# Performance work log

Measured on AMD Instinct MI355X. Metric: run time of the kernel, lower is better.

The kernel has to match this reference:

```python
import jax, jax.numpy as jnp
import numpy as np

WIN = 25            # window size (win_h == win_w == 25)
DIM = 256           # channels
DIM_HEAD = 32
HEADS = DIM // DIM_HEAD   # 8
HIDDEN = int(DIM * 2.0)   # mlp_ratio = 2.0
EPS = 1e-5


def _rel_pos_indices(w=WIN):
    # replicates the buffer built in Attention.__init__
    pos = np.arange(w)
    gi, gj = np.meshgrid(pos, pos, indexing='ij')
    grid = np.stack([gi.ravel(), gj.ravel()], axis=-1)          # (w*w, 2)
    rel = grid[:, None, :] - grid[None, :, :] + (w - 1)          # (n, n, 2)
    return jnp.asarray(rel[..., 0] * (2 * w - 1) + rel[..., 1])  # (n, n) int


def setup_inputs() -> dict:
    key = jax.random.key(0)
    ks = jax.random.split(key, 8)
    s = 0.02
    d = DIM
    return {
        'x': jax.random.normal(ks[0], (2, d, 100, 100), jnp.float32),
        'w_qkv': jax.random.normal(ks[1], (3 * d, d), jnp.float32) * s,
        'w_out': jax.random.normal(ks[2], (d, d), jnp.float32) * s,
        'rel_bias_table': jax.random.normal(ks[3], ((2 * WIN - 1) ** 2, HEADS), jnp.float32) * s,
        'gamma2': jnp.ones((d,), jnp.float32),
        'beta2': jnp.zeros((d,), jnp.float32),
        'w1': jax.random.normal(ks[4], (HIDDEN, d), jnp.float32) * s,
        'b1': jnp.zeros((HIDDEN,), jnp.float32),
        'w2': jax.random.normal(ks[5], (d, HIDDEN), jnp.float32) * s,
        'b2': jnp.zeros((d,), jnp.float32),
    }


def _layernorm(x, g, b, eps=EPS):
    m = x.mean(-1, keepdims=True)
    v = ((x - m) ** 2).mean(-1, keepdims=True)
    return (x - m) / jnp.sqrt(v + eps) * g + b


def reference(x, w_qkv, w_out, rel_bias_table, gamma2, beta2, w1, b1, w2, b2):
    b, d, H, W = x.shape
    nh, nw = H // WIN, W // WIN
    h, dh = HEADS, DIM_HEAD
    scale = dh ** -0.5
    n = WIN * WIN

    # --- window partition: (b, d, H, W) -> (b*nh*nw, n, d) ---
    xw = x.reshape(b, d, nh, WIN, nw, WIN).transpose(0, 2, 4, 3, 5, 1)
    xw = xw.reshape(b * nh * nw, n, d)

    # --- windowed attention with relative-position bias (norm1 unused in source) ---
    qkv = xw @ w_qkv.T                         # (B, n, 3d)
    q, k, v = jnp.split(qkv, 3, axis=-1)
    split_heads = lambda t: t.reshape(t.shape[0], n, h, dh).transpose(0, 2, 1, 3)
    q = split_heads(q) * scale                 # (B, h, n, dh)
    k = split_heads(k)
    v = split_heads(v)

    sim = jnp.einsum('bhid,bhjd->bhij', q, k)  # (B, h, n, n)
    bias = rel_bias_table[_rel_pos_indices()]  # (n, n, h)
    sim = sim + bias.transpose(2, 0, 1)[None]
    attn = jax.nn.softmax(sim, axis=-1)
    out = jnp.einsum('bhij,bhjd->bhid', attn, v)            # (B, h, n, dh)
    out = out.transpose(0, 2, 1, 3).reshape(-1, n, d)        # head-major concat: (m d)
    out = out @ w_out.T                                      # (B, n, d)

    # --- un-partition: (b*nh*nw, n, d) -> (b, d, H, W) ---
    xa = out.reshape(b, nh, nw, WIN, WIN, d).transpose(0, 5, 1, 3, 2, 4)
    xa = xa.reshape(b, d, H, W)

    # --- norm2 + MLP + residual ---
    y = xa.transpose(0, 2, 3, 1).reshape(b, H * W, d)
    y = _layernorm(y, gamma2, beta2)
    y = jax.nn.gelu(y @ w1.T + b1, approximate=False) @ w2.T + b2
    y = y.reshape(b, H, W, d).transpose(0, 3, 1, 2)
    return x + y
```

## Files before the change

### kernel.cpp

```cpp
#include <hip/hip_runtime.h>


using f32x4 = __attribute__((ext_vector_type(4))) float;
using s16x8 = __attribute__((ext_vector_type(8))) short;

__device__ __forceinline__ ushort f2b(float f) {
  union { float f; unsigned u; } v; v.f = f;
  return (ushort)((v.u + 0x7FFFu + ((v.u >> 16) & 1u)) >> 16);
}
__device__ __forceinline__ ushort f2b_fast(float f) {
  union { float f; unsigned u; } v; v.f = f;
  return (ushort)((v.u + 0x8000u) >> 16);
}
__device__ __forceinline__ float b2f(ushort u) {
  union { unsigned u; float f; } v; v.u = ((unsigned)u) << 16; return v.f;
}
__device__ __forceinline__ float lo2f(unsigned w) {
  union { unsigned u; float f; } v; v.u = w << 16; return v.f;
}
__device__ __forceinline__ float hi2f(unsigned w) {
  union { unsigned u; float f; } v; v.u = w & 0xffff0000u; return v.f;
}

__device__ __forceinline__ void gld16(const void* g, void* l) {
  __builtin_amdgcn_global_load_lds((const __attribute__((address_space(1))) void*)g,
                                   (__attribute__((address_space(3))) void*)l, 16, 0, 0);
}

template<int KB>
__device__ __forceinline__ void gemm_core(const ushort* __restrict__ A, int lda,
                                          const ushort* __restrict__ B, int ldb,
                                          f32x4 acc[4][4]) {
  __shared__ ushort As[128 * 64];
  __shared__ ushort Bs[128 * 64];
  const int tid = threadIdx.x;
  const int lane = tid & 63;
  const int wv = tid >> 6;
  const int wr = (wv >> 1) * 64;
  const int wc = (wv & 1) * 64;
  const int srow = (lane >> 3);
  const int sg = ((lane & 7) ^ (srow & 7)) * 8;
  f32x4 zero = {0.f, 0.f, 0.f, 0.f};
#pragma unroll
  for (int mt = 0; mt < 4; ++mt)
#pragma unroll
    for (int nt = 0; nt < 4; ++nt) acc[mt][nt] = zero;

  for (int kb = 0; kb < KB; ++kb) {
#pragma unroll
    for (int j = 0; j < 4; ++j) {
      int r0 = wv * 32 + j * 8;
      int row = r0 + srow;
      gld16(A + row * lda + kb * 64 + sg, &As[r0 * 64]);
      gld16(B + row * ldb + kb * 64 + sg, &Bs[r0 * 64]);
    }
    __syncthreads();
#pragma unroll
    for (int ks = 0; ks < 2; ++ks) {
      s16x8 af[4], bfr[4];
      const int G = ks * 4 + (lane >> 4);
#pragma unroll
      for (int mt = 0; mt < 4; ++mt) {
        int row = wr + mt * 16 + (lane & 15);
        af[mt] = *(const s16x8*)&As[row * 64 + (G ^ (row & 7)) * 8];
      }
#pragma unroll
      for (int nt = 0; nt < 4; ++nt) {
        int row = wc + nt * 16 + (lane & 15);
        bfr[nt] = *(const s16x8*)&Bs[row * 64 + (G ^ (row & 7)) * 8];
      }
#pragma unroll
      for (int mt = 0; mt < 4; ++mt)
#pragma unroll
        for (int nt = 0; nt < 4; ++nt)
          acc[mt][nt] = __builtin_amdgcn_mfma_f32_16x16x32_bf16(af[mt], bfr[nt], acc[mt][nt], 0, 0, 0);
    }
    __syncthreads();
  }
}

__global__ __launch_bounds__(256) void k_prep(const float* __restrict__ x,
                                              const float* __restrict__ wqkv,
                                              const float* __restrict__ wout,
                                              const float* __restrict__ w1,
                                              const float* __restrict__ w2,
                                              const float* __restrict__ table,
                                              ushort* __restrict__ Xw,
                                              ushort* __restrict__ wqkvb,
                                              ushort* __restrict__ woutb,
                                              ushort* __restrict__ w1b,
                                              ushort* __restrict__ w2b,
                                              ushort* __restrict__ biasPh) {
  __shared__ ushort smem[64 * 264];
  const int bid = blockIdx.x, tid = threadIdx.x;
  if (bid < 320) {
    ushort (*Ls)[264] = (ushort(*)[264])smem;
    const int t0 = bid * 64;
    const int w = t0 / 640;
    const int tokbase = t0 - w * 640;
    const int b = w >> 4, wh = (w >> 2) & 3, ww = w & 3;
    for (int i = tid; i < 64 * 256; i += 256) {
      int c = i >> 6, tl = i & 63;
      int tok = tokbase + tl;
      ushort val = 0;
      if (tok < 625) {
        int ii = tok / 25, jj = tok - ii * 25;
        val = f2b(x[((b * 256 + c) * 100 + wh * 25 + ii) * 100 + ww * 25 + jj]);
      }
      Ls[tl][c] = val;
    }
    __syncthreads();
    for (int i = tid; i < 64 * 32; i += 256) {
      int tl = i >> 5, g = (i & 31) * 8;
      *(uint4*)(Xw + (t0 + tl) * 256 + g) = *(const uint4*)&Ls[tl][g];
    }
  } else if (bid < 832) {
    int v = (bid - 320) * 1024 + tid * 4;
    const float* src; ushort* dst; int off;
    if (v < 196608)      { src = wqkv; dst = wqkvb; off = v; }
    else if (v < 262144) { src = wout; dst = woutb; off = v - 196608; }
    else if (v < 393216) { src = w1;   dst = w1b;   off = v - 262144; }
    else                 { src = w2;   dst = w2b;   off = v - 393216; }
    float4 f = *(const float4*)(src + off);
    ushort4 u; u.x = f2b(f.x); u.y = f2b(f.y); u.z = f2b(f.z); u.w = f2b(f.w);
    *(ushort4*)(dst + off) = u;
  } else {
    float* tl = (float*)smem;
    const int q = bid - 832;
    const int h = q / 40, t = q - (q / 40) * 40;
    for (int i = tid; i < 2401; i += 256) tl[i] = table[i * 8 + h] * 1.4426950408889634f;
    __syncthreads();
    const int lane = tid >> 2, rr = tid & 3;
    const int quad = lane >> 4, cl = lane & 15;
    int row = t * 16 + quad * 4 + rr;
    int rowg = (row < 625) ? row : 0;
    const int ri = rowg / 25, ci = rowg - ri * 25;
    for (int cc = 0; cc < 4; ++cc)
      for (int cp = 0; cp < 5; ++cp)
#pragma unroll
        for (int codd = 0; codd < 2; ++codd) {
          int col = cc * 160 + (cp * 2 + codd) * 16 + cl;
          float v = -1e30f;
          if (col < 625) {
            int rj = col / 25, cj = col - rj * 25;
            v = tl[(ri - rj + 24) * 49 + (ci - cj + 24)];
          }
          biasPh[((((h * 40 + t) * 4 + cc) * 5 + cp) * 64 + lane) * 8 + codd * 4 + rr] = f2b(v);
        }
  }
}

__global__ __launch_bounds__(256) void k_qkv(const ushort* __restrict__ Xw,
                                             const ushort* __restrict__ Wb,
                                             ushort* __restrict__ Qb,
                                             ushort* __restrict__ Kb,
                                             ushort* __restrict__ VbT) {
  f32x4 acc[4][4];
  gemm_core<4>(Xw + blockIdx.x * 128 * 256, 256, Wb + blockIdx.y * 128 * 256, 256, acc);
  const int lane = threadIdx.x & 63, wv = threadIdx.x >> 6;
  const int wr = (wv >> 1) * 64, wc = (wv & 1) * 64;
  const int which = blockIdx.y >> 1;
  const float QSC = 0.17677669529663687f * 1.4426950408889634f;
#pragma unroll
  for (int mt = 0; mt < 4; ++mt) {
#pragma unroll
    for (int nt = 0; nt < 4; ++nt) {
      int n = blockIdx.y * 128 + wc + nt * 16 + (lane & 15);
      int h = (n >> 5) & 7, ch = n & 31;
      int m0 = blockIdx.x * 128 + wr + mt * 16 + (lane >> 4) * 4;
      int w = m0 / 640, tok0 = m0 - w * 640;
      if (which == 2) {
        ushort4 pk;
        pk.x = f2b_fast(acc[mt][nt][0]); pk.y = f2b_fast(acc[mt][nt][1]);
        pk.z = f2b_fast(acc[mt][nt][2]); pk.w = f2b_fast(acc[mt][nt][3]);
        *(ushort4*)(VbT + (((w << 3) + h) * 32 + ch) * 640 + tok0) = pk;
      } else {
        ushort* dst = which == 0 ? Qb : Kb;
        float sc = which == 0 ? QSC : 1.f;
#pragma unroll
        for (int r = 0; r < 4; ++r)
          dst[(((w << 3) + h) * 640 + tok0 + r) * 32 + ch] = f2b_fast(acc[mt][nt][r] * sc);
      }
    }
  }
}

__global__ __launch_bounds__(256, 3) void k_attn(const ushort* __restrict__ Qb,
                                                 const ushort* __restrict__ Kb,
                                                 const ushort* __restrict__ VbT,
                                                 const ushort* __restrict__ biasPh,
                                                 ushort* __restrict__ AO) {
  __shared__ ushort Pw[4][16][164];
  const int tid = threadIdx.x;
  const int lane = tid & 63;
  const int wv = tid >> 6;
  const int quad = lane >> 4;
  const int cl = lane & 15;
  const int bid = blockIdx.x;
  const int h = bid & 7;
  const int rem = bid >> 3;
  const int win = rem / 5;
  const int tg = rem - win * 5;
  const ushort* Qg = Qb + (win * 8 + h) * 20480;
  const ushort* Kg = Kb + (win * 8 + h) * 20480;
  const ushort* Vt = VbT + (win * 8 + h) * 20480;

  const int t0 = tg * 8 + wv * 2;
  const s16x8 qf0 = *(const s16x8*)(Qg + (t0 * 16 + cl) * 32 + quad * 8);
  const s16x8 qf1 = *(const s16x8*)(Qg + ((t0 + 1) * 16 + cl) * 32 + quad * 8);
  s16x8 ones;
#pragma unroll
  for (int j = 0; j < 8; ++j) ones[j] = (short)0x3F80;

  const f32x4 zero = {0.f, 0.f, 0.f, 0.f};
  f32x4 o00 = zero, o01 = zero, o10 = zero, o11 = zero;
  f32x4 sum0 = zero, sum1 = zero;

#pragma unroll
  for (int cc = 0; cc < 4; ++cc) {
    s16x8 kf[10];
#pragma unroll
    for (int c = 0; c < 10; ++c)
      kf[c] = *(const s16x8*)(Kg + (cc * 160 + c * 16 + cl) * 32 + quad * 8);
    s16x8 vf0[5], vf1[5];
#pragma unroll
    for (int kc = 0; kc < 5; ++kc) {
      vf0[kc] = *(const s16x8*)(Vt + cl * 640 + cc * 160 + kc * 32 + quad * 8);
      vf1[kc] = *(const s16x8*)(Vt + (16 + cl) * 640 + cc * 160 + kc * 32 + quad * 8);
    }
#pragma unroll
    for (int tl = 0; tl < 2; ++tl) {
      const int t = t0 + tl;
      const s16x8 qf = tl ? qf1 : qf0;
      const ushort* bp = biasPh + (((h * 40 + t) * 4 + cc) * 5) * 512 + lane * 8;
      s16x8 bb[5];
#pragma unroll
      for (int cp = 0; cp < 5; ++cp) bb[cp] = *(const s16x8*)(bp + cp * 512);
#pragma unroll
      for (int c = 0; c < 10; ++c) {
        const unsigned* bw = (const unsigned*)&bb[c >> 1];
        const int codd = c & 1;
        f32x4 cop;
        cop[0] = lo2f(bw[codd * 2]);     cop[1] = hi2f(bw[codd * 2]);
        cop[2] = lo2f(bw[codd * 2 + 1]); cop[3] = hi2f(bw[codd * 2 + 1]);
        f32x4 sc = __builtin_amdgcn_mfma_f32_16x16x32_bf16(qf, kf[c], cop, 0, 0, 0);
#pragma unroll
        for (int r = 0; r < 4; ++r)
          Pw[wv][quad * 4 + r][c * 16 + cl] = f2b_fast(exp2f(sc[r]));
      }
      f32x4& o0 = tl ? o10 : o00;
      f32x4& o1 = tl ? o11 : o01;
      f32x4& sm = tl ? sum1 : sum0;
#pragma unroll
      for (int kc = 0; kc < 5; ++kc) {
        s16x8 pf = *(const s16x8*)&Pw[wv][cl][kc * 32 + quad * 8];
        o0 = __builtin_amdgcn_mfma_f32_16x16x32_bf16(pf, vf0[kc], o0, 0, 0, 0);
        o1 = __builtin_amdgcn_mfma_f32_16x16x32_bf16(pf, vf1[kc], o1, 0, 0, 0);
        sm = __builtin_amdgcn_mfma_f32_16x16x32_bf16(pf, ones, sm, 0, 0, 0);
      }
    }
  }
#pragma unroll
  for (int tl = 0; tl < 2; ++tl) {
    const f32x4& o0 = tl ? o10 : o00;
    const f32x4& o1 = tl ? o11 : o01;
    const f32x4& sm = tl ? sum1 : sum0;
#pragma unroll
    for (int r = 0; r < 4; ++r) {
      float inv = 1.f / sm[r];
      int tok = (t0 + tl) * 16 + quad * 4 + r;
      if (tok < 625) {
        int base = (win * 640 + tok) * 256 + h * 32;
        AO[base + cl] = f2b_fast(o0[r] * inv);
        AO[base + 16 + cl] = f2b_fast(o1[r] * inv);
      }
    }
  }
}

__global__ __launch_bounds__(256, 2) void k_out_ln(const ushort* __restrict__ AO,
                                                   const ushort* __restrict__ Wb,
                                                   const float* __restrict__ gamma,
                                                   const float* __restrict__ beta,
                                                   ushort* __restrict__ Yn) {
  __shared__ ushort As[64 * 64];
  __shared__ ushort Bs[256 * 64];
  __shared__ float red[2][64][2];
  const int tid = threadIdx.x;
  const int lane = tid & 63;
  const int wv = tid >> 6;
  const int wr = (wv >> 1) * 32, wc = (wv & 1) * 128;
  const int quad = lane >> 4, cl = lane & 15;
  const int srow = lane >> 3;
  const int sg = ((lane & 7) ^ (srow & 7)) * 8;
  f32x4 zero = {0.f, 0.f, 0.f, 0.f};
  f32x4 acc[2][8];
#pragma unroll
  for (int mt = 0; mt < 2; ++mt)
#pragma unroll
    for (int nt = 0; nt < 8; ++nt) acc[mt][nt] = zero;

  const ushort* A = AO + blockIdx.x * 64 * 256;
  for (int kb = 0; kb < 4; ++kb) {
#pragma unroll
    for (int i = 0; i < 10; ++i) {
      int r0 = (wv + i * 4) * 8;
      int row = r0 + srow;
      if (r0 < 64) gld16(A + row * 256 + kb * 64 + sg, &As[r0 * 64]);
      else         gld16(Wb + (row - 64) * 256 + kb * 64 + sg, &Bs[(r0 - 64) * 64]);
    }
    __syncthreads();
#pragma unroll
    for (int ks = 0; ks < 2; ++ks) {
      s16x8 af[2], bfr[8];
      const int G = ks * 4 + quad;
#pragma unroll
      for (int mt = 0; mt < 2; ++mt) {
        int row = wr + mt * 16 + cl;
        af[mt] = *(const s16x8*)&As[row * 64 + (G ^ (row & 7)) * 8];
      }
#pragma unroll
      for (int nt = 0; nt < 8; ++nt) {
        int row = wc + nt * 16 + cl;
        bfr[nt] = *(const s16x8*)&Bs[row * 64 + (G ^ (row & 7)) * 8];
      }
#pragma unroll
      for (int mt = 0; mt < 2; ++mt)
#pragma unroll
        for (int nt = 0; nt < 8; ++nt)
          acc[mt][nt] = __builtin_amdgcn_mfma_f32_16x16x32_bf16(af[mt], bfr[nt], acc[mt][nt], 0, 0, 0);
    }
    __syncthreads();
  }
#pragma unroll
  for (int mt = 0; mt < 2; ++mt)
#pragma unroll
    for (int r = 0; r < 4; ++r) {
      float s = 0.f, ss = 0.f;
#pragma unroll
      for (int nt = 0; nt < 8; ++nt) { float v = acc[mt][nt][r]; s += v; ss += v * v; }
      s += __shfl_xor(s, 1, 64); ss += __shfl_xor(ss, 1, 64);
      s += __shfl_xor(s, 2, 64); ss += __shfl_xor(ss, 2, 64);
      s += __shfl_xor(s, 4, 64); ss += __shfl_xor(ss, 4, 64);
      s += __shfl_xor(s, 8, 64); ss += __shfl_xor(ss, 8, 64);
      if (cl == 0) {
        int row = wr + mt * 16 + quad * 4 + r;
        red[wc >> 7][row][0] = s;
        red[wc >> 7][row][1] = ss;
      }
    }
  __syncthreads();
  float g[8], bt[8];
#pragma unroll
  for (int nt = 0; nt < 8; ++nt) { int n = wc + nt * 16 + cl; g[nt] = gamma[n]; bt[nt] = beta[n]; }
  const int m0 = blockIdx.x * 64;
#pragma unroll
  for (int mt = 0; mt < 2; ++mt)
#pragma unroll
    for (int r = 0; r < 4; ++r) {
      int row = wr + mt * 16 + quad * 4 + r;
      int m = m0 + row;
      int w = m / 640, tok = m - w * 640;
      if (tok < 625) {
        float sum = red[0][row][0] + red[1][row][0];
        float ssum = red[0][row][1] + red[1][row][1];
        float mean = sum * 0.00390625f;
        float var = ssum * 0.00390625f - mean * mean;
        float rstd = rsqrtf(var + 1e-5f);
        int b = w >> 4, whh = (w >> 2) & 3, www = w & 3;
        int ii = tok / 25, jj = tok - ii * 25;
        int p = (whh * 25 + ii) * 100 + www * 25 + jj;
        ushort* dst = Yn + (b * 10000 + p) * 256;
#pragma unroll
        for (int nt = 0; nt < 8; ++nt) {
          float v = (acc[mt][nt][r] - mean) * rstd * g[nt] + bt[nt];
          dst[wc + nt * 16 + cl] = f2b_fast(v);
        }
      }
    }
}

__global__ __launch_bounds__(256) void k_fc1(const ushort* __restrict__ Yn,
                                             const ushort* __restrict__ W1b,
                                             const float* __restrict__ b1,
                                             ushort* __restrict__ G) {
  f32x4 acc[4][4];
  gemm_core<4>(Yn + blockIdx.x * 128 * 256, 256, W1b + blockIdx.y * 128 * 256, 256, acc);
  const int lane = threadIdx.x & 63, wv = threadIdx.x >> 6;
  const int wr = (wv >> 1) * 64, wc = (wv & 1) * 64;
#pragma unroll
  for (int mt = 0; mt < 4; ++mt)
#pragma unroll
    for (int nt = 0; nt < 4; ++nt) {
      int n = blockIdx.y * 128 + wc + nt * 16 + (lane & 15);
      float bias = b1[n];
#pragma unroll
      for (int r = 0; r < 4; ++r) {
        int m = blockIdx.x * 128 + wr + mt * 16 + (lane >> 4) * 4 + r;
        float v = acc[mt][nt][r] + bias;
        v = 0.5f * v * (1.f + erff(v * 0.70710678118f));
        G[m * 512 + n] = f2b_fast(v);
      }
    }
}

__global__ __launch_bounds__(256) void k_fc2(const ushort* __restrict__ W2b,
                                             const ushort* __restrict__ G,
                                             const float* __restrict__ b2,
                                             const float* __restrict__ x,
                                             float* __restrict__ out) {
  __shared__ ushort As[64 * 64];
  __shared__ ushort Bs[128 * 64];
  const int tid = threadIdx.x;
  const int lane = tid & 63;
  const int wv = tid >> 6;
  const int wr = (wv >> 1) * 32;
  const int wc = (wv & 1) * 64;
  const int quad = lane >> 4, cl = lane & 15;
  const int srow = lane >> 3;
  const int sg = ((lane & 7) ^ (srow & 7)) * 8;
  f32x4 zero = {0.f, 0.f, 0.f, 0.f};
  f32x4 acc[2][4];
#pragma unroll
  for (int mt = 0; mt < 2; ++mt)
#pragma unroll
    for (int nt = 0; nt < 4; ++nt) acc[mt][nt] = zero;

  const ushort* A = W2b + blockIdx.x * 64 * 512;
  const ushort* B = G + blockIdx.y * 128 * 512;
  for (int kb = 0; kb < 8; ++kb) {
#pragma unroll
    for (int j = 0; j < 2; ++j) {
      int r0 = (wv * 2 + j) * 8;
      gld16(A + (r0 + srow) * 512 + kb * 64 + sg, &As[r0 * 64]);
    }
#pragma unroll
    for (int j = 0; j < 4; ++j) {
      int r0 = (wv * 4 + j) * 8;
      gld16(B + (r0 + srow) * 512 + kb * 64 + sg, &Bs[r0 * 64]);
    }
    __syncthreads();
#pragma unroll
    for (int ks = 0; ks < 2; ++ks) {
      s16x8 af[2], bfr[4];
      const int Gx = ks * 4 + quad;
#pragma unroll
      for (int mt = 0; mt < 2; ++mt) {
        int row = wr + mt * 16 + cl;
        af[mt] = *(const s16x8*)&As[row * 64 + (Gx ^ (row & 7)) * 8];
      }
#pragma unroll
      for (int nt = 0; nt < 4; ++nt) {
        int row = wc + nt * 16 + cl;
        bfr[nt] = *(const s16x8*)&Bs[row * 64 + (Gx ^ (row & 7)) * 8];
      }
#pragma unroll
      for (int mt = 0; mt < 2; ++mt)
#pragma unroll
        for (int nt = 0; nt < 4; ++nt)
          acc[mt][nt] = __builtin_amdgcn_mfma_f32_16x16x32_bf16(af[mt], bfr[nt], acc[mt][nt], 0, 0, 0);
    }
    __syncthreads();
  }
#pragma unroll
  for (int mt = 0; mt < 2; ++mt)
#pragma unroll
    for (int nt = 0; nt < 4; ++nt) {
      int t = blockIdx.y * 128 + wc + nt * 16 + cl;
      if (t < 20000) {
        int b = t / 10000, p = t - b * 10000;
#pragma unroll
        for (int r = 0; r < 4; ++r) {
          int c = blockIdx.x * 64 + wr + mt * 16 + quad * 4 + r;
          int idx = (b * 256 + c) * 10000 + p;
          out[idx] = x[idx] + acc[mt][nt][r] + b2[c];
        }
      }
    }
}

extern "C" void kernel_launch(void* const* d_in, const int* in_sizes, int n_in,
                              void* d_out, int out_size, void* d_ws, size_t ws_size,
                              hipStream_t stream) {
  const float* x     = (const float*)d_in[0];
  const float* wqkv  = (const float*)d_in[1];
  const float* wout  = (const float*)d_in[2];
  const float* bias  = (const float*)d_in[3];
  const float* gamma = (const float*)d_in[4];
  const float* beta  = (const float*)d_in[5];
  const float* w1    = (const float*)d_in[6];
  const float* b1    = (const float*)d_in[7];
  const float* w2    = (const float*)d_in[8];
  const float* b2    = (const float*)d_in[9];
  float* out = (float*)d_out;
  char* ws = (char*)d_ws;

  ushort* Xw    = (ushort*)(ws + 0);
  ushort* AO    = Xw;
  ushort* wqkvb = (ushort*)(ws + 10485760);
  ushort* woutb = (ushort*)(ws + 10878976);
  ushort* w1b   = (ushort*)(ws + 11010048);
  ushort* w2b   = (ushort*)(ws + 11272192);
  ushort* Qb    = (ushort*)(ws + 11534336);
  ushort* Kb    = (ushort*)(ws + 22020096);
  ushort* VbT   = (ushort*)(ws + 32505856);
  ushort* biasPh= (ushort*)(ws + 42991616);
  ushort* Yn    = (ushort*)(ws + 22020096);
  ushort* G     = (ushort*)(ws + 32505856);

  k_prep  <<<1152, 256, 0, stream>>>(x, wqkv, wout, w1, w2, bias,
                                     Xw, wqkvb, woutb, w1b, w2b, biasPh);
  k_qkv   <<<dim3(160, 6), 256, 0, stream>>>(Xw, wqkvb, Qb, Kb, VbT);
  k_attn  <<<1280, 256, 0, stream>>>(Qb, Kb, VbT, biasPh, AO);
  k_out_ln<<<320, 256, 0, stream>>>(AO, woutb, gamma, beta, Yn);
  k_fc1   <<<dim3(157, 4), 256, 0, stream>>>(Yn, w1b, b1, G);
  k_fc2   <<<dim3(4, 157), 256, 0, stream>>>(w2b, G, b2, x, out);
}
```

Before: 230.8 us.

## Double-buffer LDS tiles in GEMM cores and raise attention occupancy bound

Both the shared GEMM core and the fc2 kernel now keep two LDS tile buffers. The next K-tile is loaded asynchronously while MFMAs run on the current one, and one barrier per iteration is dropped. This aims to hide global-to-LDS latency behind compute, at the cost of twice the shared memory per block, which can lower occupancy. The attention kernel's launch bounds also rise from 3 to 4 blocks per CU, which may force register spills.

```diff
diff --git a/kernel.cpp b/kernel.cpp
--- a/kernel.cpp
+++ b/kernel.cpp
@@ -31,8 +31,8 @@
 __device__ __forceinline__ void gemm_core(const ushort* __restrict__ A, int lda,
                                           const ushort* __restrict__ B, int ldb,
                                           f32x4 acc[4][4]) {
-  __shared__ ushort As[128 * 64];
-  __shared__ ushort Bs[128 * 64];
+  __shared__ ushort As[2][128 * 64];
+  __shared__ ushort Bs[2][128 * 64];
   const int tid = threadIdx.x;
   const int lane = tid & 63;
   const int wv = tid >> 6;
@@ -46,15 +46,26 @@
 #pragma unroll
     for (int nt = 0; nt < 4; ++nt) acc[mt][nt] = zero;
 
+#pragma unroll
+  for (int j = 0; j < 4; ++j) {
+    int r0 = wv * 32 + j * 8;
+    int row = r0 + srow;
+    gld16(A + row * lda + sg, &As[0][r0 * 64]);
+    gld16(B + row * ldb + sg, &Bs[0][r0 * 64]);
+  }
   for (int kb = 0; kb < KB; ++kb) {
-#pragma unroll
-    for (int j = 0; j < 4; ++j) {
-      int r0 = wv * 32 + j * 8;
-      int row = r0 + srow;
-      gld16(A + row * lda + kb * 64 + sg, &As[r0 * 64]);
-      gld16(B + row * ldb + kb * 64 + sg, &Bs[r0 * 64]);
-    }
     __syncthreads();
+    if (kb + 1 < KB) {
+      const int nb = (kb + 1) & 1;
+#pragma unroll
+      for (int j = 0; j < 4; ++j) {
+        int r0 = wv * 32 + j * 8;
+        int row = r0 + srow;
+        gld16(A + row * lda + (kb + 1) * 64 + sg, &As[nb][r0 * 64]);
+        gld16(B + row * ldb + (kb + 1) * 64 + sg, &Bs[nb][r0 * 64]);
+      }
+    }
+    const int cb = kb & 1;
 #pragma unroll
     for (int ks = 0; ks < 2; ++ks) {
       s16x8 af[4], bfr[4];
@@ -62,12 +73,12 @@
 #pragma unroll
       for (int mt = 0; mt < 4; ++mt) {
         int row = wr + mt * 16 + (lane & 15);
-        af[mt] = *(const s16x8*)&As[row * 64 + (G ^ (row & 7)) * 8];
+        af[mt] = *(const s16x8*)&As[cb][row * 64 + (G ^ (row & 7)) * 8];
       }
 #pragma unroll
       for (int nt = 0; nt < 4; ++nt) {
         int row = wc + nt * 16 + (lane & 15);
-        bfr[nt] = *(const s16x8*)&Bs[row * 64 + (G ^ (row & 7)) * 8];
+        bfr[nt] = *(const s16x8*)&Bs[cb][row * 64 + (G ^ (row & 7)) * 8];
       }
 #pragma unroll
       for (int mt = 0; mt < 4; ++mt)
@@ -75,7 +86,6 @@
         for (int nt = 0; nt < 4; ++nt)
           acc[mt][nt] = __builtin_amdgcn_mfma_f32_16x16x32_bf16(af[mt], bfr[nt], acc[mt][nt], 0, 0, 0);
     }
-    __syncthreads();
   }
 }
 
@@ -185,7 +195,7 @@
   }
 }
 
-__global__ __launch_bounds__(256, 3) void k_attn(const ushort* __restrict__ Qb,
+__global__ __launch_bounds__(256, 4) void k_attn(const ushort* __restrict__ Qb,
                                                  const ushort* __restrict__ Kb,
                                                  const ushort* __restrict__ VbT,
                                                  const ushort* __restrict__ biasPh,
@@ -409,8 +419,8 @@
                                              const float* __restrict__ b2,
                                              const float* __restrict__ x,
                                              float* __restrict__ out) {
-  __shared__ ushort As[64 * 64];
-  __shared__ ushort Bs[128 * 64];
+  __shared__ ushort As[2][64 * 64];
+  __shared__ ushort Bs[2][128 * 64];
   const int tid = threadIdx.x;
   const int lane = tid & 63;
   const int wv = tid >> 6;
@@ -428,18 +438,32 @@
 
   const ushort* A = W2b + blockIdx.x * 64 * 512;
   const ushort* B = G + blockIdx.y * 128 * 512;
+#pragma unroll
+  for (int j = 0; j < 2; ++j) {
+    int r0 = (wv * 2 + j) * 8;
+    gld16(A + (r0 + srow) * 512 + sg, &As[0][r0 * 64]);
+  }
+#pragma unroll
+  for (int j = 0; j < 4; ++j) {
+    int r0 = (wv * 4 + j) * 8;
+    gld16(B + (r0 + srow) * 512 + sg, &Bs[0][r0 * 64]);
+  }
   for (int kb = 0; kb < 8; ++kb) {
-#pragma unroll
-    for (int j = 0; j < 2; ++j) {
-      int r0 = (wv * 2 + j) * 8;
-      gld16(A + (r0 + srow) * 512 + kb * 64 + sg, &As[r0 * 64]);
-    }
-#pragma unroll
-    for (int j = 0; j < 4; ++j) {
-      int r0 = (wv * 4 + j) * 8;
-      gld16(B + (r0 + srow) * 512 + kb * 64 + sg, &Bs[r0 * 64]);
-    }
     __syncthreads();
+    if (kb + 1 < 8) {
+      const int nb = (kb + 1) & 1;
+#pragma unroll
+      for (int j = 0; j < 2; ++j) {
+        int r0 = (wv * 2 + j) * 8;
+        gld16(A + (r0 + srow) * 512 + (kb + 1) * 64 + sg, &As[nb][r0 * 64]);
+      }
+#pragma unroll
+      for (int j = 0; j < 4; ++j) {
+        int r0 = (wv * 4 + j) * 8;
+        gld16(B + (r0 + srow) * 512 + (kb + 1) * 64 + sg, &Bs[nb][r0 * 64]);
+      }
+    }
+    const int cb = kb & 1;
 #pragma unroll
     for (int ks = 0; ks < 2; ++ks) {
       s16x8 af[2], bfr[4];
@@ -447,12 +471,12 @@
 #pragma unroll
       for (int mt = 0; mt < 2; ++mt) {
         int row = wr + mt * 16 + cl;
-        af[mt] = *(const s16x8*)&As[row * 64 + (Gx ^ (row & 7)) * 8];
+        af[mt] = *(const s16x8*)&As[cb][row * 64 + (Gx ^ (row & 7)) * 8];
       }
 #pragma unroll
       for (int nt = 0; nt < 4; ++nt) {
         int row = wc + nt * 16 + cl;
-        bfr[nt] = *(const s16x8*)&Bs[row * 64 + (Gx ^ (row & 7)) * 8];
+        bfr[nt] = *(const s16x8*)&Bs[cb][row * 64 + (Gx ^ (row & 7)) * 8];
       }
 #pragma unroll
       for (int mt = 0; mt < 2; ++mt)
@@ -460,7 +484,6 @@
         for (int nt = 0; nt < 4; ++nt)
           acc[mt][nt] = __builtin_amdgcn_mfma_f32_16x16x32_bf16(af[mt], bfr[nt], acc[mt][nt], 0, 0, 0);
     }
-    __syncthreads();
   }
 #pragma unroll
   for (int mt = 0; mt < 2; ++mt)
```

Result: slower. 259.3 us (+12.4%).

## Fuse out-projection, layernorm and fc1+GELU into one kernel via LDS tile

Applied to the files above, without the earlier changes.

Merges the output projection with layernorm and the first MLP layer: the normalized 64x256 tile stays in shared memory as bf16 and is multiplied by W1 in four 128-column chunks, with the GELU output scattered straight to image-order rows of G. This removes the Yn round trip through global memory and one kernel launch. In exchange each block streams all of W1, runs the fc1 GEMM at smaller per-block tiles, and uses about 34KB more shared memory, which may cut occupancy. The variance is also clamped at zero before rsqrt.

```diff
diff --git a/kernel.cpp b/kernel.cpp
--- a/kernel.cpp
+++ b/kernel.cpp
@@ -11,9 +11,6 @@
 __device__ __forceinline__ ushort f2b_fast(float f) {
   union { float f; unsigned u; } v; v.f = f;
   return (ushort)((v.u + 0x8000u) >> 16);
-}
-__device__ __forceinline__ float b2f(ushort u) {
-  union { unsigned u; float f; } v; v.u = ((unsigned)u) << 16; return v.f;
 }
 __device__ __forceinline__ float lo2f(unsigned w) {
   union { unsigned u; float f; } v; v.u = w << 16; return v.f;
@@ -278,130 +275,172 @@
   }
 }
 
-__global__ __launch_bounds__(256, 2) void k_out_ln(const ushort* __restrict__ AO,
-                                                   const ushort* __restrict__ Wb,
-                                                   const float* __restrict__ gamma,
-                                                   const float* __restrict__ beta,
-                                                   ushort* __restrict__ Yn) {
+__global__ __launch_bounds__(256, 2) void k_out_mlp(const ushort* __restrict__ AO,
+                                                    const ushort* __restrict__ Wb,
+                                                    const float* __restrict__ gamma,
+                                                    const float* __restrict__ beta,
+                                                    const ushort* __restrict__ W1b,
+                                                    const float* __restrict__ b1,
+                                                    ushort* __restrict__ G) {
   __shared__ ushort As[64 * 64];
   __shared__ ushort Bs[256 * 64];
   __shared__ float red[2][64][2];
+  __shared__ ushort Yt[64][264];
+  __shared__ int gpL[64];
   const int tid = threadIdx.x;
   const int lane = tid & 63;
   const int wv = tid >> 6;
-  const int wr = (wv >> 1) * 32, wc = (wv & 1) * 128;
   const int quad = lane >> 4, cl = lane & 15;
   const int srow = lane >> 3;
   const int sg = ((lane & 7) ^ (srow & 7)) * 8;
   f32x4 zero = {0.f, 0.f, 0.f, 0.f};
-  f32x4 acc[2][8];
-#pragma unroll
-  for (int mt = 0; mt < 2; ++mt)
-#pragma unroll
-    for (int nt = 0; nt < 8; ++nt) acc[mt][nt] = zero;
-
-  const ushort* A = AO + blockIdx.x * 64 * 256;
-  for (int kb = 0; kb < 4; ++kb) {
-#pragma unroll
-    for (int i = 0; i < 10; ++i) {
-      int r0 = (wv + i * 4) * 8;
-      int row = r0 + srow;
-      if (r0 < 64) gld16(A + row * 256 + kb * 64 + sg, &As[r0 * 64]);
-      else         gld16(Wb + (row - 64) * 256 + kb * 64 + sg, &Bs[(r0 - 64) * 64]);
-    }
-    __syncthreads();
-#pragma unroll
-    for (int ks = 0; ks < 2; ++ks) {
-      s16x8 af[2], bfr[8];
-      const int G = ks * 4 + quad;
-#pragma unroll
-      for (int mt = 0; mt < 2; ++mt) {
-        int row = wr + mt * 16 + cl;
-        af[mt] = *(const s16x8*)&As[row * 64 + (G ^ (row & 7)) * 8];
-      }
-#pragma unroll
-      for (int nt = 0; nt < 8; ++nt) {
-        int row = wc + nt * 16 + cl;
-        bfr[nt] = *(const s16x8*)&Bs[row * 64 + (G ^ (row & 7)) * 8];
-      }
-#pragma unroll
-      for (int mt = 0; mt < 2; ++mt)
-#pragma unroll
-        for (int nt = 0; nt < 8; ++nt)
-          acc[mt][nt] = __builtin_amdgcn_mfma_f32_16x16x32_bf16(af[mt], bfr[nt], acc[mt][nt], 0, 0, 0);
-    }
-    __syncthreads();
-  }
-#pragma unroll
-  for (int mt = 0; mt < 2; ++mt)
-#pragma unroll
-    for (int r = 0; r < 4; ++r) {
-      float s = 0.f, ss = 0.f;
-#pragma unroll
-      for (int nt = 0; nt < 8; ++nt) { float v = acc[mt][nt][r]; s += v; ss += v * v; }
-      s += __shfl_xor(s, 1, 64); ss += __shfl_xor(ss, 1, 64);
-      s += __shfl_xor(s, 2, 64); ss += __shfl_xor(ss, 2, 64);
-      s += __shfl_xor(s, 4, 64); ss += __shfl_xor(ss, 4, 64);
-      s += __shfl_xor(s, 8, 64); ss += __shfl_xor(ss, 8, 64);
-      if (cl == 0) {
+
+  {
+    const int wr = (wv >> 1) * 32, wc = (wv & 1) * 128;
+    f32x4 acc[2][8];
+#pragma unroll
+    for (int mt = 0; mt < 2; ++mt)
+#pragma unroll
+      for (int nt = 0; nt < 8; ++nt) acc[mt][nt] = zero;
+
+    const ushort* A = AO + blockIdx.x * 64 * 256;
+    for (int kb = 0; kb < 4; ++kb) {
+#pragma unroll
+      for (int i = 0; i < 10; ++i) {
+        int r0 = (wv + i * 4) * 8;
+        int row = r0 + srow;
+        if (r0 < 64) gld16(A + row * 256 + kb * 64 + sg, &As[r0 * 64]);
+        else         gld16(Wb + (row - 64) * 256 + kb * 64 + sg, &Bs[(r0 - 64) * 64]);
+      }
+      __syncthreads();
+#pragma unroll
+      for (int ks = 0; ks < 2; ++ks) {
+        s16x8 af[2], bfr[8];
+        const int Gx = ks * 4 + quad;
+#pragma unroll
+        for (int mt = 0; mt < 2; ++mt) {
+          int row = wr + mt * 16 + cl;
+          af[mt] = *(const s16x8*)&As[row * 64 + (Gx ^ (row & 7)) * 8];
+        }
+#pragma unroll
+        for (int nt = 0; nt < 8; ++nt) {
+          int row = wc + nt * 16 + cl;
+          bfr[nt] = *(const s16x8*)&Bs[row * 64 + (Gx ^ (row & 7)) * 8];
+        }
+#pragma unroll
+        for (int mt = 0; mt < 2; ++mt)
+#pragma unroll
+          for (int nt = 0; nt < 8; ++nt)
+            acc[mt][nt] = __builtin_amdgcn_mfma_f32_16x16x32_bf16(af[mt], bfr[nt], acc[mt][nt], 0, 0, 0);
+      }
+      __syncthreads();
+    }
+#pragma unroll
+    for (int mt = 0; mt < 2; ++mt)
+#pragma unroll
+      for (int r = 0; r < 4; ++r) {
+        float s = 0.f, ss = 0.f;
+#pragma unroll
+        for (int nt = 0; nt < 8; ++nt) { float v = acc[mt][nt][r]; s += v; ss += v * v; }
+        s += __shfl_xor(s, 1, 64); ss += __shfl_xor(ss, 1, 64);
+        s += __shfl_xor(s, 2, 64); ss += __shfl_xor(ss, 2, 64);
+        s += __shfl_xor(s, 4, 64); ss += __shfl_xor(ss, 4, 64);
+        s += __shfl_xor(s, 8, 64); ss += __shfl_xor(ss, 8, 64);
+        if (cl == 0) {
+          int row = wr + mt * 16 + quad * 4 + r;
+          red[wc >> 7][row][0] = s;
+          red[wc >> 7][row][1] = ss;
+        }
+      }
+    __syncthreads();
+    float g[8], bt[8];
+#pragma unroll
+    for (int nt = 0; nt < 8; ++nt) { int n = wc + nt * 16 + cl; g[nt] = gamma[n]; bt[nt] = beta[n]; }
+    const int m0 = blockIdx.x * 64;
+#pragma unroll
+    for (int mt = 0; mt < 2; ++mt)
+#pragma unroll
+      for (int r = 0; r < 4; ++r) {
         int row = wr + mt * 16 + quad * 4 + r;
-        red[wc >> 7][row][0] = s;
-        red[wc >> 7][row][1] = ss;
-      }
-    }
-  __syncthreads();
-  float g[8], bt[8];
-#pragma unroll
-  for (int nt = 0; nt < 8; ++nt) { int n = wc + nt * 16 + cl; g[nt] = gamma[n]; bt[nt] = beta[n]; }
-  const int m0 = blockIdx.x * 64;
-#pragma unroll
-  for (int mt = 0; mt < 2; ++mt)
-#pragma unroll
-    for (int r = 0; r < 4; ++r) {
-      int row = wr + mt * 16 + quad * 4 + r;
-      int m = m0 + row;
-      int w = m / 640, tok = m - w * 640;
-      if (tok < 625) {
         float sum = red[0][row][0] + red[1][row][0];
         float ssum = red[0][row][1] + red[1][row][1];
         float mean = sum * 0.00390625f;
         float var = ssum * 0.00390625f - mean * mean;
-        float rstd = rsqrtf(var + 1e-5f);
-        int b = w >> 4, whh = (w >> 2) & 3, www = w & 3;
-        int ii = tok / 25, jj = tok - ii * 25;
-        int p = (whh * 25 + ii) * 100 + www * 25 + jj;
-        ushort* dst = Yn + (b * 10000 + p) * 256;
+        float rstd = rsqrtf(fmaxf(var, 0.f) + 1e-5f);
 #pragma unroll
         for (int nt = 0; nt < 8; ++nt) {
           float v = (acc[mt][nt][r] - mean) * rstd * g[nt] + bt[nt];
-          dst[wc + nt * 16 + cl] = f2b_fast(v);
-        }
-      }
-    }
-}
-
-__global__ __launch_bounds__(256) void k_fc1(const ushort* __restrict__ Yn,
-                                             const ushort* __restrict__ W1b,
-                                             const float* __restrict__ b1,
-                                             ushort* __restrict__ G) {
-  f32x4 acc[4][4];
-  gemm_core<4>(Yn + blockIdx.x * 128 * 256, 256, W1b + blockIdx.y * 128 * 256, 256, acc);
-  const int lane = threadIdx.x & 63, wv = threadIdx.x >> 6;
-  const int wr = (wv >> 1) * 64, wc = (wv & 1) * 64;
-#pragma unroll
-  for (int mt = 0; mt < 4; ++mt)
-#pragma unroll
-    for (int nt = 0; nt < 4; ++nt) {
-      int n = blockIdx.y * 128 + wc + nt * 16 + (lane & 15);
-      float bias = b1[n];
-#pragma unroll
-      for (int r = 0; r < 4; ++r) {
-        int m = blockIdx.x * 128 + wr + mt * 16 + (lane >> 4) * 4 + r;
-        float v = acc[mt][nt][r] + bias;
-        v = 0.5f * v * (1.f + erff(v * 0.70710678118f));
-        G[m * 512 + n] = f2b_fast(v);
-      }
-    }
+          Yt[row][wc + nt * 16 + cl] = f2b_fast(v);
+        }
+        if (cl == 0 && wc == 0) {
+          int m = m0 + row;
+          int w = m / 640, tok = m - w * 640;
+          int gp = -1;
+          if (tok < 625) {
+            int b = w >> 4, whh = (w >> 2) & 3, www = w & 3;
+            int ii = tok / 25, jj = tok - ii * 25;
+            gp = b * 10000 + (whh * 25 + ii) * 100 + www * 25 + jj;
+          }
+          gpL[row] = gp;
+        }
+      }
+  }
+  {
+    const int wr = (wv >> 1) * 32, wc = (wv & 1) * 64;
+    for (int nb = 0; nb < 4; ++nb) {
+      f32x4 acc2[2][4];
+#pragma unroll
+      for (int mt = 0; mt < 2; ++mt)
+#pragma unroll
+        for (int nt = 0; nt < 4; ++nt) acc2[mt][nt] = zero;
+      for (int kb = 0; kb < 4; ++kb) {
+#pragma unroll
+        for (int j = 0; j < 4; ++j) {
+          int r0 = (wv * 4 + j) * 8;
+          gld16(W1b + (nb * 128 + r0 + srow) * 256 + kb * 64 + sg, &Bs[r0 * 64]);
+        }
+        __syncthreads();
+#pragma unroll
+        for (int ks = 0; ks < 2; ++ks) {
+          s16x8 af[2], bfr[4];
+          const int Gx = ks * 4 + quad;
+#pragma unroll
+          for (int mt = 0; mt < 2; ++mt) {
+            int row = wr + mt * 16 + cl;
+            af[mt] = *(const s16x8*)&Yt[row][kb * 64 + ks * 32 + quad * 8];
+          }
+#pragma unroll
+          for (int nt = 0; nt < 4; ++nt) {
+            int row = wc + nt * 16 + cl;
+            bfr[nt] = *(const s16x8*)&Bs[row * 64 + (Gx ^ (row & 7)) * 8];
+          }
+#pragma unroll
+          for (int mt = 0; mt < 2; ++mt)
+#pragma unroll
+            for (int nt = 0; nt < 4; ++nt)
+              acc2[mt][nt] = __builtin_amdgcn_mfma_f32_16x16x32_bf16(af[mt], bfr[nt], acc2[mt][nt], 0, 0, 0);
+        }
+        __syncthreads();
+      }
+#pragma unroll
+      for (int mt = 0; mt < 2; ++mt)
+#pragma unroll
+        for (int nt = 0; nt < 4; ++nt) {
+          int n = nb * 128 + wc + nt * 16 + cl;
+          float bias = b1[n];
+#pragma unroll
+          for (int r = 0; r < 4; ++r) {
+            int row = wr + mt * 16 + quad * 4 + r;
+            int gp = gpL[row];
+            if (gp >= 0) {
+              float v = acc2[mt][nt][r] + bias;
+              v = 0.5f * v * (1.f + erff(v * 0.70710678118f));
+              G[gp * 512 + n] = f2b_fast(v);
+            }
+          }
+        }
+    }
+  }
 }
 
 __global__ __launch_bounds__(256) void k_fc2(const ushort* __restrict__ W2b,
@@ -505,14 +544,12 @@
   ushort* Kb    = (ushort*)(ws + 22020096);
   ushort* VbT   = (ushort*)(ws + 32505856);
   ushort* biasPh= (ushort*)(ws + 42991616);
-  ushort* Yn    = (ushort*)(ws + 22020096);
   ushort* G     = (ushort*)(ws + 32505856);
 
-  k_prep  <<<1152, 256, 0, stream>>>(x, wqkv, wout, w1, w2, bias,
-                                     Xw, wqkvb, woutb, w1b, w2b, biasPh);
-  k_qkv   <<<dim3(160, 6), 256, 0, stream>>>(Xw, wqkvb, Qb, Kb, VbT);
-  k_attn  <<<1280, 256, 0, stream>>>(Qb, Kb, VbT, biasPh, AO);
-  k_out_ln<<<320, 256, 0, stream>>>(AO, woutb, gamma, beta, Yn);
-  k_fc1   <<<dim3(157, 4), 256, 0, stream>>>(Yn, w1b, b1, G);
-  k_fc2   <<<dim3(4, 157), 256, 0, stream>>>(w2b, G, b2, x, out);
-}
+  k_prep   <<<1152, 256, 0, stream>>>(x, wqkv, wout, w1, w2, bias,
+                                      Xw, wqkvb, woutb, w1b, w2b, biasPh);
+  k_qkv    <<<dim3(160, 6), 256, 0, stream>>>(Xw, wqkvb, Qb, Kb, VbT);
+  k_attn   <<<1280, 256, 0, stream>>>(Qb, Kb, VbT, biasPh, AO);
+  k_out_mlp<<<320, 256, 0, stream>>>(AO, woutb, gamma, beta, w1b, b1, G);
+  k_fc2    <<<dim3(4, 157), 256, 0, stream>>>(w2b, G, b2, x, out);
+}
```

Measured after the change: 236.0 us. 1.02x slower.
